# Kernel tuning notes

Measured on AMD Instinct MI355X. Metric: run time of the kernel, lower is better.

## Reference

```python
import jax, jax.numpy as jnp
import numpy as np

EPS = 1e-4

B, H, T, DH = 4, 16, 4096, 64
NF = 256


def _gaussian_orthogonal_random_matrix(rng, n_rows, n_cols):
    # Stacked orthogonal blocks from QR of gaussian blocks, scaled by row norms
    n_full = n_rows // n_cols
    blocks = []
    for _ in range(n_full):
        g = rng.standard_normal((n_cols, n_cols)).astype(np.float32)
        q, _ = np.linalg.qr(g)
        blocks.append(q.T)
    rem = n_rows - n_full * n_cols
    if rem > 0:
        g = rng.standard_normal((n_cols, n_cols)).astype(np.float32)
        q, _ = np.linalg.qr(g)
        blocks.append(q.T[:rem])
    final = np.concatenate(blocks, axis=0)
    multiplier = np.linalg.norm(rng.standard_normal((n_rows, n_cols)).astype(np.float32), axis=1)
    return (multiplier[:, None] * final).astype(np.float32)


def setup_inputs() -> dict:
    key = jax.random.key(0)
    kq, kk, kv = jax.random.split(key, 3)
    q = jax.random.normal(kq, (B, H, T, DH), dtype=jnp.float32)
    k = jax.random.normal(kk, (B, H, T, DH), dtype=jnp.float32)
    v = jax.random.normal(kv, (B, H, T, DH), dtype=jnp.float32)
    proj = jnp.asarray(_gaussian_orthogonal_random_matrix(np.random.default_rng(0), NF, DH))
    return {"q": q, "k": k, "v": v, "projection_matrix": proj}


def _softmax_kernel(data, proj, is_query):
    # data: [B,H,T,Dh], proj: [NF,Dh]
    data_scale = data.shape[-1] ** -0.25
    scale = proj.shape[0] ** -0.5
    dp = jnp.einsum('bhid,jd->bhij', data_scale * data, proj)  # [B,H,T,NF]
    dn = (jnp.sum(data ** 2, axis=-1) * (0.5 * data_scale ** 2))[..., None]
    axes = (-1, -2) if is_query else (-1,)
    m = jax.lax.stop_gradient(jnp.max(dp, axis=axes, keepdims=True))
    return scale * jnp.exp(dp - dn - m + EPS)


def reference(q, k, v, projection_matrix):
    qp = _softmax_kernel(q, projection_matrix, True)   # [B,H,T,NF]
    kp = _softmax_kernel(k, projection_matrix, False)  # [B,H,T,NF]
    context = jnp.einsum('bhnd,bhne->bhde', kp, v)     # [B,H,NF,Dh]
    d_inv = 1.0 / jnp.einsum('bhnd,bhd->bhn', qp, kp.sum(axis=-2))
    out = jnp.einsum('bhde,bhnd,bhn->bhne', context, qp, d_inv)
    return out
```

## Files before the change

kernel.cpp:

```cpp
#include <hip/hip_runtime.h>

typedef _Float16 f16;
typedef __attribute__((ext_vector_type(4))) _Float16 f16x4;
typedef __attribute__((ext_vector_type(8))) _Float16 f16x8;
typedef __attribute__((ext_vector_type(4))) float f32x4;

#define Tn 4096
#define DHn 64
#define NFn 256
#define BHn 64
#define TCH 64
#define NCH 8
#define TBLK (TCH * NCH)
#define GRIDX (Tn / TBLK)
#define KLD 72
#define WLDA 72
#define WLDB 264
#define CTXF (65 * NFn)

static constexpr float L2E  = 1.4426950408889634f;
static constexpr float DS   = 0.35355339059327379f;
static constexpr float DSL  = 0.35355339059327379f * 1.4426950408889634f;
static constexpr float DNS2 = 0.0625f * 1.4426950408889634f;
static constexpr float SH2  = 12.0f * 1.4426950408889634f;

__device__ __forceinline__ float fexp2(float x) { return __builtin_amdgcn_exp2f(x); }

#define BAR() do { asm volatile("s_waitcnt lgkmcnt(0)" ::: "memory"); \
                   __builtin_amdgcn_s_barrier(); } while (0)

__global__ __launch_bounds__(256, 2)
void perf_ctx_mfma(const float* __restrict__ K, const float* __restrict__ V,
                   const float* __restrict__ P, float* __restrict__ ctxws,
                   float* __restrict__ part, int use_part)
{
    __shared__ __align__(16) f16 kLDS[TCH * KLD];
    __shared__ __align__(16) f16 vT[2][DHn * KLD];
    __shared__ __align__(16) f16 wLDS[NFn * WLDA];
    __shared__ float dn[TCH];
    __shared__ __align__(16) float redmax[TCH][4];

    const int bh   = blockIdx.y;
    const int tid  = threadIdx.x;
    const int lane = tid & 63;
    const int wv   = tid >> 6;
    const int c    = lane & 15;
    const int g    = lane >> 4;

    f16x8 pb[4][2];
#pragma unroll
    for (int nt = 0; nt < 4; nt++)
#pragma unroll
        for (int kc = 0; kc < 2; kc++) {
            const float* s = P + (size_t)(64 * wv + 16 * nt + c) * DHn + 32 * kc + 8 * g;
            f16x8 h;
#pragma unroll
            for (int j = 0; j < 8; j++) h[j] = (f16)(s[j] * DSL);
            pb[nt][kc] = h;
        }

    f32x4 cacc[4][4];
#pragma unroll
    for (int a = 0; a < 4; a++)
#pragma unroll
        for (int b = 0; b < 4; b++) cacc[a][b] = (f32x4){0.f, 0.f, 0.f, 0.f};
    float sp[4] = {0.f, 0.f, 0.f, 0.f};

    const float* Kb = K + (size_t)bh * Tn * DHn;
    const float* Vb = V + (size_t)bh * Tn * DHn;
    const int rb = 4 * wv + g;

    float4 kq[4], vq[4], kqn[4], vqn[4];
    {
        const int t0 = blockIdx.x * TBLK;
#pragma unroll
        for (int i = 0; i < 4; i++) {
            const int r = 16 * i + rb;
            kq[i] = *(const float4*)(Kb + (size_t)(t0 + r) * DHn + 4 * c);
            vq[i] = *(const float4*)(Vb + (size_t)(t0 + r) * DHn + 4 * c);
        }
    }

    for (int ch = 0; ch < NCH; ch++) {
        f16* vTc = &vT[ch & 1][0];
#pragma unroll
        for (int i = 0; i < 4; i++) {
            const int r = 16 * i + rb;
            f16x4 hk;
            hk[0] = (f16)kq[i].x; hk[1] = (f16)kq[i].y;
            hk[2] = (f16)kq[i].z; hk[3] = (f16)kq[i].w;
            *(f16x4*)&kLDS[r * KLD + 4 * c] = hk;
            float p = kq[i].x * kq[i].x + kq[i].y * kq[i].y +
                      kq[i].z * kq[i].z + kq[i].w * kq[i].w;
            p += __shfl_xor(p, 1); p += __shfl_xor(p, 2);
            p += __shfl_xor(p, 4); p += __shfl_xor(p, 8);
            if (c == 0) dn[r] = p * DNS2;
            const float* vf = &vq[i].x;
#pragma unroll
            for (int m = 0; m < 4; m++) {
                const int dh = 4 * c + m;
                vTc[dh * KLD + ((((r >> 3) ^ ((dh >> 3) & 7)) << 3) | (r & 7))] = (f16)vf[m];
            }
        }
        if (ch + 1 < NCH) {
            const int t1 = blockIdx.x * TBLK + (ch + 1) * TCH;
#pragma unroll
            for (int i = 0; i < 4; i++) {
                const int r = 16 * i + rb;
                kqn[i] = *(const float4*)(Kb + (size_t)(t1 + r) * DHn + 4 * c);
                vqn[i] = *(const float4*)(Vb + (size_t)(t1 + r) * DHn + 4 * c);
            }
        }
        BAR();

        f32x4 dp[4][4];
#pragma unroll
        for (int a = 0; a < 4; a++)
#pragma unroll
            for (int b = 0; b < 4; b++) dp[a][b] = (f32x4){0.f, 0.f, 0.f, 0.f};
        __builtin_amdgcn_s_setprio(1);
#pragma unroll
        for (int mt = 0; mt < 4; mt++) {
            const f16x8 a0 = *(const f16x8*)&kLDS[(16 * mt + c) * KLD + 8 * g];
            const f16x8 a1 = *(const f16x8*)&kLDS[(16 * mt + c) * KLD + 32 + 8 * g];
#pragma unroll
            for (int nt = 0; nt < 4; nt++) {
                dp[mt][nt] = __builtin_amdgcn_mfma_f32_16x16x32_f16(a0, pb[nt][0], dp[mt][nt], 0, 0, 0);
                dp[mt][nt] = __builtin_amdgcn_mfma_f32_16x16x32_f16(a1, pb[nt][1], dp[mt][nt], 0, 0, 0);
            }
        }
        __builtin_amdgcn_s_setprio(0);
#pragma unroll
        for (int mt = 0; mt < 4; mt++)
#pragma unroll
            for (int r = 0; r < 4; r++) {
                float m = fmaxf(fmaxf(dp[mt][0][r], dp[mt][1][r]),
                                fmaxf(dp[mt][2][r], dp[mt][3][r]));
                m = fmaxf(m, __shfl_xor(m, 1)); m = fmaxf(m, __shfl_xor(m, 2));
                m = fmaxf(m, __shfl_xor(m, 4)); m = fmaxf(m, __shfl_xor(m, 8));
                if (c == 0) redmax[16 * mt + 4 * g + r][wv] = m;
            }
        BAR();

#pragma unroll
        for (int mt = 0; mt < 4; mt++) {
            float mx[4];
#pragma unroll
            for (int r = 0; r < 4; r++) {
                const int t = 16 * mt + 4 * g + r;
                const f32x4 rm = *(const f32x4*)&redmax[t][0];
                mx[r] = fmaxf(fmaxf(rm[0], rm[1]), fmaxf(rm[2], rm[3])) + dn[t];
            }
#pragma unroll
            for (int nt = 0; nt < 4; nt++) {
                f16x4 hw;
#pragma unroll
                for (int r = 0; r < 4; r++) {
                    const float w = fexp2(dp[mt][nt][r] - mx[r]);
                    sp[nt] += w;
                    hw[r] = (f16)w;
                }
                *(f16x4*)&wLDS[(64 * wv + 16 * nt + c) * WLDA + 16 * mt + 4 * g] = hw;
            }
        }
        BAR();

        __builtin_amdgcn_s_setprio(1);
#pragma unroll
        for (int kc = 0; kc < 2; kc++) {
            f16x8 af[4], bf[4];
#pragma unroll
            for (int mt2 = 0; mt2 < 4; mt2++)
                af[mt2] = *(const f16x8*)&wLDS[(64 * wv + 16 * mt2 + c) * WLDA + 32 * kc + 8 * g];
#pragma unroll
            for (int nt2 = 0; nt2 < 4; nt2++) {
                const int dh = 16 * nt2 + c;
                const int tb = 4 * kc + g;
                bf[nt2] = *(const f16x8*)&vTc[dh * KLD + ((tb ^ ((dh >> 3) & 7)) << 3)];
            }
#pragma unroll
            for (int mt2 = 0; mt2 < 4; mt2++)
#pragma unroll
                for (int nt2 = 0; nt2 < 4; nt2++)
                    cacc[mt2][nt2] = __builtin_amdgcn_mfma_f32_16x16x32_f16(
                        af[mt2], bf[nt2], cacc[mt2][nt2], 0, 0, 0);
        }
        __builtin_amdgcn_s_setprio(0);
#pragma unroll
        for (int i = 0; i < 4; i++) { kq[i] = kqn[i]; vq[i] = vqn[i]; }
    }

    if (use_part) {
        float* pb2 = part + (size_t)(bh * GRIDX + blockIdx.x) * CTXF;
#pragma unroll
        for (int mt2 = 0; mt2 < 4; mt2++)
#pragma unroll
            for (int nt2 = 0; nt2 < 4; nt2++)
                *(f32x4*)&pb2[(size_t)(16 * nt2 + c) * NFn + 64 * wv + 16 * mt2 + 4 * g] =
                    cacc[mt2][nt2];
#pragma unroll
        for (int nt = 0; nt < 4; nt++) {
            float sv = sp[nt];
            sv += __shfl_xor(sv, 16); sv += __shfl_xor(sv, 32);
            if (g == 0) pb2[64 * NFn + 64 * wv + 16 * nt + c] = sv;
        }
    } else {
        float* cb = ctxws + (size_t)bh * CTXF;
#pragma unroll
        for (int mt2 = 0; mt2 < 4; mt2++)
#pragma unroll
            for (int nt2 = 0; nt2 < 4; nt2++)
#pragma unroll
                for (int r = 0; r < 4; r++)
                    atomicAdd(&cb[(size_t)(16 * nt2 + c) * NFn + 64 * wv + 16 * mt2 + 4 * g + r],
                              cacc[mt2][nt2][r]);
#pragma unroll
        for (int nt = 0; nt < 4; nt++) {
            float sv = sp[nt];
            sv += __shfl_xor(sv, 16); sv += __shfl_xor(sv, 32);
            if (g == 0) atomicAdd(&cb[64 * NFn + 64 * wv + 16 * nt + c], sv);
        }
    }
}

__global__ __launch_bounds__(256)
void perf_reduce(const float* __restrict__ part, float* __restrict__ ctxws)
{
    const int bh = blockIdx.y;
    const float* p0 = part + (size_t)bh * GRIDX * CTXF;
    float* cb = ctxws + (size_t)bh * CTXF;
    for (int j = 4 * (threadIdx.x + 256 * blockIdx.x); j < CTXF; j += 4 * 256 * 8) {
        float4 a = *(const float4*)(p0 + j);
#pragma unroll
        for (int s = 1; s < GRIDX; s++) {
            const float4 b4 = *(const float4*)(p0 + (size_t)s * CTXF + j);
            a.x += b4.x; a.y += b4.y; a.z += b4.z; a.w += b4.w;
        }
        *(float4*)(cb + j) = a;
    }
}

__global__ __launch_bounds__(256, 2)
void perf_out_mfma(const float* __restrict__ Q, const float* __restrict__ P,
                   const float* __restrict__ ctxws, float* __restrict__ Out)
{
    __shared__ __align__(16) f16 qLDS[TCH * KLD];
    __shared__ __align__(16) f16 wLDS[TCH * WLDB];
    __shared__ __align__(16) f16 ctxLDS[DHn * WLDB];
    __shared__ float sLDS[NFn];
    __shared__ __align__(16) float denP[TCH][4];

    const int bh   = blockIdx.y;
    const int tid  = threadIdx.x;
    const int lane = tid & 63;
    const int wv   = tid >> 6;
    const int c    = lane & 15;
    const int g    = lane >> 4;

    const float* Qb = Q + (size_t)bh * Tn * DHn;
    float* Ob = Out + (size_t)bh * Tn * DHn;
    const int rb = 4 * wv + g;

    float4 qv[4], qvn[4];
    {
        const int t0 = blockIdx.x * TBLK;
#pragma unroll
        for (int i = 0; i < 4; i++)
            qv[i] = *(const float4*)(Qb + (size_t)(t0 + 16 * i + rb) * DHn + 4 * c);
    }

    f16x8 pb[4][2];
#pragma unroll
    for (int nt = 0; nt < 4; nt++)
#pragma unroll
        for (int kc = 0; kc < 2; kc++) {
            const float* s = P + (size_t)(64 * wv + 16 * nt + c) * DHn + 32 * kc + 8 * g;
            f16x8 h;
#pragma unroll
            for (int j = 0; j < 8; j++) h[j] = (f16)(s[j] * DSL);
            pb[nt][kc] = h;
        }

    const float* cb = ctxws + (size_t)bh * CTXF;
    {
        const int dh = tid >> 2;
        const int nq = (tid & 3) * 64;
#pragma unroll
        for (int u = 0; u < 16; u++) {
            const float4 cv = *(const float4*)&cb[(size_t)dh * NFn + nq + 4 * u];
            const float* cf = &cv.x;
#pragma unroll
            for (int i = 0; i < 4; i++) {
                const int ct = nq + 4 * u + i;
                const int cs = (ct & ~63) | ((ct & 15) << 2) | ((ct >> 4) & 3);
                ctxLDS[dh * WLDB + cs] = (f16)cf[i];
            }
        }
        sLDS[tid] = cb[64 * NFn + tid];
    }
    BAR();
    float s4[4];
#pragma unroll
    for (int nt = 0; nt < 4; nt++) s4[nt] = sLDS[64 * wv + 16 * nt + c];

    for (int ch = 0; ch < NCH; ch++) {
        const int t0 = blockIdx.x * TBLK + ch * TCH;
#pragma unroll
        for (int i = 0; i < 4; i++) {
            const int r = 16 * i + rb;
            f16x4 h;
            h[0] = (f16)qv[i].x; h[1] = (f16)qv[i].y;
            h[2] = (f16)qv[i].z; h[3] = (f16)qv[i].w;
            *(f16x4*)&qLDS[r * KLD + 4 * c] = h;
        }
        if (ch + 1 < NCH) {
            const int t1 = blockIdx.x * TBLK + (ch + 1) * TCH;
#pragma unroll
            for (int i = 0; i < 4; i++)
                qvn[i] = *(const float4*)(Qb + (size_t)(t1 + 16 * i + rb) * DHn + 4 * c);
        }
        BAR();

        f32x4 dp[4][4];
#pragma unroll
        for (int a = 0; a < 4; a++)
#pragma unroll
            for (int b = 0; b < 4; b++) dp[a][b] = (f32x4){0.f, 0.f, 0.f, 0.f};
        __builtin_amdgcn_s_setprio(1);
#pragma unroll
        for (int mt = 0; mt < 4; mt++) {
            const f16x8 a0 = *(const f16x8*)&qLDS[(16 * mt + c) * KLD + 8 * g];
            const f16x8 a1 = *(const f16x8*)&qLDS[(16 * mt + c) * KLD + 32 + 8 * g];
#pragma unroll
            for (int nt = 0; nt < 4; nt++) {
                dp[mt][nt] = __builtin_amdgcn_mfma_f32_16x16x32_f16(a0, pb[nt][0], dp[mt][nt], 0, 0, 0);
                dp[mt][nt] = __builtin_amdgcn_mfma_f32_16x16x32_f16(a1, pb[nt][1], dp[mt][nt], 0, 0, 0);
            }
        }
        __builtin_amdgcn_s_setprio(0);

#pragma unroll
        for (int mt = 0; mt < 4; mt++) {
#pragma unroll
            for (int r = 0; r < 4; r++) {
                const float w0 = fexp2(dp[mt][0][r] - SH2);
                const float w1 = fexp2(dp[mt][1][r] - SH2);
                const float w2 = fexp2(dp[mt][2][r] - SH2);
                const float w3 = fexp2(dp[mt][3][r] - SH2);
                float d = w0 * s4[0] + w1 * s4[1] + w2 * s4[2] + w3 * s4[3];
                d += __shfl_xor(d, 1); d += __shfl_xor(d, 2);
                d += __shfl_xor(d, 4); d += __shfl_xor(d, 8);
                const int t = 16 * mt + 4 * g + r;
                if (c == 0) denP[t][wv] = d;
                f16x4 hw;
                hw[0] = (f16)w0; hw[1] = (f16)w1; hw[2] = (f16)w2; hw[3] = (f16)w3;
                *(f16x4*)&wLDS[t * WLDB + 64 * wv + 4 * c] = hw;
            }
        }
        BAR();

        f32x4 oacc[4];
#pragma unroll
        for (int nt2 = 0; nt2 < 4; nt2++) oacc[nt2] = (f32x4){0.f, 0.f, 0.f, 0.f};
        __builtin_amdgcn_s_setprio(1);
#pragma unroll
        for (int kc = 0; kc < 8; kc++) {
            const f16x8 a = *(const f16x8*)&wLDS[(16 * wv + c) * WLDB + 32 * kc + 8 * g];
#pragma unroll
            for (int nt2 = 0; nt2 < 4; nt2++) {
                const f16x8 b = *(const f16x8*)&ctxLDS[(16 * nt2 + c) * WLDB + 32 * kc + 8 * g];
                oacc[nt2] = __builtin_amdgcn_mfma_f32_16x16x32_f16(a, b, oacc[nt2], 0, 0, 0);
            }
        }
        __builtin_amdgcn_s_setprio(0);
#pragma unroll
        for (int r = 0; r < 4; r++) {
            const int t = 16 * wv + 4 * g + r;
            const f32x4 d4 = *(const f32x4*)&denP[t][0];
            const float dinv = __builtin_amdgcn_rcpf(d4[0] + d4[1] + d4[2] + d4[3]);
#pragma unroll
            for (int nt2 = 0; nt2 < 4; nt2++)
                Ob[(size_t)(t0 + t) * DHn + 16 * nt2 + c] = oacc[nt2][r] * dinv;
        }
        BAR();
#pragma unroll
        for (int i = 0; i < 4; i++) qv[i] = qvn[i];
    }
}

extern "C" void kernel_launch(void* const* d_in, const int* in_sizes, int n_in,
                              void* d_out, int out_size, void* d_ws, size_t ws_size,
                              hipStream_t stream) {
    const float* q    = (const float*)d_in[0];
    const float* k    = (const float*)d_in[1];
    const float* v    = (const float*)d_in[2];
    const float* proj = (const float*)d_in[3];
    float* out = (float*)d_out;
    float* ctx = (float*)d_ws;

    (void)in_sizes; (void)n_in; (void)out_size;

    const size_t ctx_bytes  = (size_t)BHn * CTXF * sizeof(float);
    const size_t part_bytes = (size_t)BHn * GRIDX * CTXF * sizeof(float);
    const int use_part = (ws_size >= ctx_bytes + part_bytes) ? 1 : 0;
    float* part = ctx + (size_t)BHn * CTXF;

    if (!use_part)
        hipMemsetAsync(ctx, 0, ctx_bytes, stream);
    perf_ctx_mfma<<<dim3(GRIDX, BHn), 256, 0, stream>>>(k, v, proj, ctx, part, use_part);
    if (use_part)
        perf_reduce<<<dim3(8, BHn), 256, 0, stream>>>(part, ctx);
    perf_out_mfma<<<dim3(GRIDX, BHn), 256, 0, stream>>>(q, proj, ctx, out);
}
```

Measured before the change: 268.6 us.

## Double workgroup size to 8 waves, splitting feature columns across waves

```diff
diff --git a/kernel.cpp b/kernel.cpp
--- a/kernel.cpp
+++ b/kernel.cpp
@@ -1,6 +1,7 @@
 #include <hip/hip_runtime.h>
 
 typedef _Float16 f16;
+typedef __attribute__((ext_vector_type(2))) _Float16 f16x2;
 typedef __attribute__((ext_vector_type(4))) _Float16 f16x4;
 typedef __attribute__((ext_vector_type(8))) _Float16 f16x8;
 typedef __attribute__((ext_vector_type(4))) float f32x4;
@@ -18,8 +19,6 @@
 #define WLDB 264
 #define CTXF (65 * NFn)
 
-static constexpr float L2E  = 1.4426950408889634f;
-static constexpr float DS   = 0.35355339059327379f;
 static constexpr float DSL  = 0.35355339059327379f * 1.4426950408889634f;
 static constexpr float DNS2 = 0.0625f * 1.4426950408889634f;
 static constexpr float SH2  = 12.0f * 1.4426950408889634f;
@@ -29,7 +28,7 @@
 #define BAR() do { asm volatile("s_waitcnt lgkmcnt(0)" ::: "memory"); \
                    __builtin_amdgcn_s_barrier(); } while (0)
 
-__global__ __launch_bounds__(256, 2)
+__global__ __launch_bounds__(512, 4)
 void perf_ctx_mfma(const float* __restrict__ K, const float* __restrict__ V,
                    const float* __restrict__ P, float* __restrict__ ctxws,
                    float* __restrict__ part, int use_part)
@@ -38,7 +37,7 @@
     __shared__ __align__(16) f16 vT[2][DHn * KLD];
     __shared__ __align__(16) f16 wLDS[NFn * WLDA];
     __shared__ float dn[TCH];
-    __shared__ __align__(16) float redmax[TCH][4];
+    __shared__ __align__(16) float redmax[TCH][8];
 
     const int bh   = blockIdx.y;
     const int tid  = threadIdx.x;
@@ -47,35 +46,35 @@
     const int c    = lane & 15;
     const int g    = lane >> 4;
 
-    f16x8 pb[4][2];
-#pragma unroll
-    for (int nt = 0; nt < 4; nt++)
+    f16x8 pb[2][2];
+#pragma unroll
+    for (int nt = 0; nt < 2; nt++)
 #pragma unroll
         for (int kc = 0; kc < 2; kc++) {
-            const float* s = P + (size_t)(64 * wv + 16 * nt + c) * DHn + 32 * kc + 8 * g;
+            const float* s = P + (size_t)(32 * wv + 16 * nt + c) * DHn + 32 * kc + 8 * g;
             f16x8 h;
 #pragma unroll
             for (int j = 0; j < 8; j++) h[j] = (f16)(s[j] * DSL);
             pb[nt][kc] = h;
         }
 
-    f32x4 cacc[4][4];
-#pragma unroll
-    for (int a = 0; a < 4; a++)
+    f32x4 cacc[2][4];
+#pragma unroll
+    for (int a = 0; a < 2; a++)
 #pragma unroll
         for (int b = 0; b < 4; b++) cacc[a][b] = (f32x4){0.f, 0.f, 0.f, 0.f};
-    float sp[4] = {0.f, 0.f, 0.f, 0.f};
+    float sp[2] = {0.f, 0.f};
 
     const float* Kb = K + (size_t)bh * Tn * DHn;
     const float* Vb = V + (size_t)bh * Tn * DHn;
-    const int rb = 4 * wv + g;
-
-    float4 kq[4], vq[4], kqn[4], vqn[4];
+    const int rb = tid >> 4;
+
+    float4 kq[2], vq[2], kqn[2], vqn[2];
     {
         const int t0 = blockIdx.x * TBLK;
 #pragma unroll
-        for (int i = 0; i < 4; i++) {
-            const int r = 16 * i + rb;
+        for (int i = 0; i < 2; i++) {
+            const int r = 32 * i + rb;
             kq[i] = *(const float4*)(Kb + (size_t)(t0 + r) * DHn + 4 * c);
             vq[i] = *(const float4*)(Vb + (size_t)(t0 + r) * DHn + 4 * c);
         }
@@ -84,8 +83,8 @@
     for (int ch = 0; ch < NCH; ch++) {
         f16* vTc = &vT[ch & 1][0];
 #pragma unroll
-        for (int i = 0; i < 4; i++) {
-            const int r = 16 * i + rb;
+        for (int i = 0; i < 2; i++) {
+            const int r = 32 * i + rb;
             f16x4 hk;
             hk[0] = (f16)kq[i].x; hk[1] = (f16)kq[i].y;
             hk[2] = (f16)kq[i].z; hk[3] = (f16)kq[i].w;
@@ -105,26 +104,26 @@
         if (ch + 1 < NCH) {
             const int t1 = blockIdx.x * TBLK + (ch + 1) * TCH;
 #pragma unroll
-            for (int i = 0; i < 4; i++) {
-                const int r = 16 * i + rb;
+            for (int i = 0; i < 2; i++) {
+                const int r = 32 * i + rb;
                 kqn[i] = *(const float4*)(Kb + (size_t)(t1 + r) * DHn + 4 * c);
                 vqn[i] = *(const float4*)(Vb + (size_t)(t1 + r) * DHn + 4 * c);
             }
         }
         BAR();
 
-        f32x4 dp[4][4];
+        f32x4 dp[4][2];
 #pragma unroll
         for (int a = 0; a < 4; a++)
 #pragma unroll
-            for (int b = 0; b < 4; b++) dp[a][b] = (f32x4){0.f, 0.f, 0.f, 0.f};
+            for (int b = 0; b < 2; b++) dp[a][b] = (f32x4){0.f, 0.f, 0.f, 0.f};
         __builtin_amdgcn_s_setprio(1);
 #pragma unroll
         for (int mt = 0; mt < 4; mt++) {
             const f16x8 a0 = *(const f16x8*)&kLDS[(16 * mt + c) * KLD + 8 * g];
             const f16x8 a1 = *(const f16x8*)&kLDS[(16 * mt + c) * KLD + 32 + 8 * g];
 #pragma unroll
-            for (int nt = 0; nt < 4; nt++) {
+            for (int nt = 0; nt < 2; nt++) {
                 dp[mt][nt] = __builtin_amdgcn_mfma_f32_16x16x32_f16(a0, pb[nt][0], dp[mt][nt], 0, 0, 0);
                 dp[mt][nt] = __builtin_amdgcn_mfma_f32_16x16x32_f16(a1, pb[nt][1], dp[mt][nt], 0, 0, 0);
             }
@@ -134,8 +133,7 @@
         for (int mt = 0; mt < 4; mt++)
 #pragma unroll
             for (int r = 0; r < 4; r++) {
-                float m = fmaxf(fmaxf(dp[mt][0][r], dp[mt][1][r]),
-                                fmaxf(dp[mt][2][r], dp[mt][3][r]));
+                float m = fmaxf(dp[mt][0][r], dp[mt][1][r]);
                 m = fmaxf(m, __shfl_xor(m, 1)); m = fmaxf(m, __shfl_xor(m, 2));
                 m = fmaxf(m, __shfl_xor(m, 4)); m = fmaxf(m, __shfl_xor(m, 8));
                 if (c == 0) redmax[16 * mt + 4 * g + r][wv] = m;
@@ -148,11 +146,13 @@
 #pragma unroll
             for (int r = 0; r < 4; r++) {
                 const int t = 16 * mt + 4 * g + r;
-                const f32x4 rm = *(const f32x4*)&redmax[t][0];
-                mx[r] = fmaxf(fmaxf(rm[0], rm[1]), fmaxf(rm[2], rm[3])) + dn[t];
-            }
-#pragma unroll
-            for (int nt = 0; nt < 4; nt++) {
+                const f32x4 r0 = *(const f32x4*)&redmax[t][0];
+                const f32x4 r1 = *(const f32x4*)&redmax[t][4];
+                mx[r] = fmaxf(fmaxf(fmaxf(r0[0], r0[1]), fmaxf(r0[2], r0[3])),
+                              fmaxf(fmaxf(r1[0], r1[1]), fmaxf(r1[2], r1[3]))) + dn[t];
+            }
+#pragma unroll
+            for (int nt = 0; nt < 2; nt++) {
                 f16x4 hw;
 #pragma unroll
                 for (int r = 0; r < 4; r++) {
@@ -160,7 +160,7 @@
                     sp[nt] += w;
                     hw[r] = (f16)w;
                 }
-                *(f16x4*)&wLDS[(64 * wv + 16 * nt + c) * WLDA + 16 * mt + 4 * g] = hw;
+                *(f16x4*)&wLDS[(32 * wv + 16 * nt + c) * WLDA + 16 * mt + 4 * g] = hw;
             }
         }
         BAR();
@@ -168,10 +168,10 @@
         __builtin_amdgcn_s_setprio(1);
 #pragma unroll
         for (int kc = 0; kc < 2; kc++) {
-            f16x8 af[4], bf[4];
-#pragma unroll
-            for (int mt2 = 0; mt2 < 4; mt2++)
-                af[mt2] = *(const f16x8*)&wLDS[(64 * wv + 16 * mt2 + c) * WLDA + 32 * kc + 8 * g];
+            f16x8 af[2], bf[4];
+#pragma unroll
+            for (int mt2 = 0; mt2 < 2; mt2++)
+                af[mt2] = *(const f16x8*)&wLDS[(32 * wv + 16 * mt2 + c) * WLDA + 32 * kc + 8 * g];
 #pragma unroll
             for (int nt2 = 0; nt2 < 4; nt2++) {
                 const int dh = 16 * nt2 + c;
@@ -179,7 +179,7 @@
                 bf[nt2] = *(const f16x8*)&vTc[dh * KLD + ((tb ^ ((dh >> 3) & 7)) << 3)];
             }
 #pragma unroll
-            for (int mt2 = 0; mt2 < 4; mt2++)
+            for (int mt2 = 0; mt2 < 2; mt2++)
 #pragma unroll
                 for (int nt2 = 0; nt2 < 4; nt2++)
                     cacc[mt2][nt2] = __builtin_amdgcn_mfma_f32_16x16x32_f16(
@@ -187,38 +187,38 @@
         }
         __builtin_amdgcn_s_setprio(0);
 #pragma unroll
-        for (int i = 0; i < 4; i++) { kq[i] = kqn[i]; vq[i] = vqn[i]; }
+        for (int i = 0; i < 2; i++) { kq[i] = kqn[i]; vq[i] = vqn[i]; }
     }
 
     if (use_part) {
         float* pb2 = part + (size_t)(bh * GRIDX + blockIdx.x) * CTXF;
 #pragma unroll
-        for (int mt2 = 0; mt2 < 4; mt2++)
+        for (int mt2 = 0; mt2 < 2; mt2++)
 #pragma unroll
             for (int nt2 = 0; nt2 < 4; nt2++)
-                *(f32x4*)&pb2[(size_t)(16 * nt2 + c) * NFn + 64 * wv + 16 * mt2 + 4 * g] =
+                *(f32x4*)&pb2[(size_t)(16 * nt2 + c) * NFn + 32 * wv + 16 * mt2 + 4 * g] =
                     cacc[mt2][nt2];
 #pragma unroll
-        for (int nt = 0; nt < 4; nt++) {
+        for (int nt = 0; nt < 2; nt++) {
             float sv = sp[nt];
             sv += __shfl_xor(sv, 16); sv += __shfl_xor(sv, 32);
-            if (g == 0) pb2[64 * NFn + 64 * wv + 16 * nt + c] = sv;
+            if (g == 0) pb2[64 * NFn + 32 * wv + 16 * nt + c] = sv;
         }
     } else {
         float* cb = ctxws + (size_t)bh * CTXF;
 #pragma unroll
-        for (int mt2 = 0; mt2 < 4; mt2++)
+        for (int mt2 = 0; mt2 < 2; mt2++)
 #pragma unroll
             for (int nt2 = 0; nt2 < 4; nt2++)
 #pragma unroll
                 for (int r = 0; r < 4; r++)
-                    atomicAdd(&cb[(size_t)(16 * nt2 + c) * NFn + 64 * wv + 16 * mt2 + 4 * g + r],
+                    atomicAdd(&cb[(size_t)(16 * nt2 + c) * NFn + 32 * wv + 16 * mt2 + 4 * g + r],
                               cacc[mt2][nt2][r]);
 #pragma unroll
-        for (int nt = 0; nt < 4; nt++) {
+        for (int nt = 0; nt < 2; nt++) {
             float sv = sp[nt];
             sv += __shfl_xor(sv, 16); sv += __shfl_xor(sv, 32);
-            if (g == 0) atomicAdd(&cb[64 * NFn + 64 * wv + 16 * nt + c], sv);
+            if (g == 0) atomicAdd(&cb[64 * NFn + 32 * wv + 16 * nt + c], sv);
         }
     }
 }
@@ -240,7 +240,7 @@
     }
 }
 
-__global__ __launch_bounds__(256, 2)
+__global__ __launch_bounds__(512, 4)
 void perf_out_mfma(const float* __restrict__ Q, const float* __restrict__ P,
                    const float* __restrict__ ctxws, float* __restrict__ Out)
 {
@@ -248,7 +248,7 @@
     __shared__ __align__(16) f16 wLDS[TCH * WLDB];
     __shared__ __align__(16) f16 ctxLDS[DHn * WLDB];
     __shared__ float sLDS[NFn];
-    __shared__ __align__(16) float denP[TCH][4];
+    __shared__ __align__(16) float denP[TCH][8];
 
     const int bh   = blockIdx.y;
     const int tid  = threadIdx.x;
@@ -259,22 +259,22 @@
 
     const float* Qb = Q + (size_t)bh * Tn * DHn;
     float* Ob = Out + (size_t)bh * Tn * DHn;
-    const int rb = 4 * wv + g;
-
-    float4 qv[4], qvn[4];
+    const int rb = tid >> 4;
+
+    float4 qv[2], qvn[2];
     {
         const int t0 = blockIdx.x * TBLK;
 #pragma unroll
-        for (int i = 0; i < 4; i++)
-            qv[i] = *(const float4*)(Qb + (size_t)(t0 + 16 * i + rb) * DHn + 4 * c);
-    }
-
-    f16x8 pb[4][2];
-#pragma unroll
-    for (int nt = 0; nt < 4; nt++)
+        for (int i = 0; i < 2; i++)
+            qv[i] = *(const float4*)(Qb + (size_t)(t0 + 32 * i + rb) * DHn + 4 * c);
+    }
+
+    f16x8 pb[2][2];
+#pragma unroll
+    for (int nt = 0; nt < 2; nt++)
 #pragma unroll
         for (int kc = 0; kc < 2; kc++) {
-            const float* s = P + (size_t)(64 * wv + 16 * nt + c) * DHn + 32 * kc + 8 * g;
+            const float* s = P + (size_t)(32 * wv + 16 * nt + c) * DHn + 32 * kc + 8 * g;
             f16x8 h;
 #pragma unroll
             for (int j = 0; j < 8; j++) h[j] = (f16)(s[j] * DSL);
@@ -283,31 +283,34 @@
 
     const float* cb = ctxws + (size_t)bh * CTXF;
     {
-        const int dh = tid >> 2;
-        const int nq = (tid & 3) * 64;
-#pragma unroll
-        for (int u = 0; u < 16; u++) {
+        const int dh = tid >> 3;
+        const int nq = (tid & 7) * 32;
+#pragma unroll
+        for (int u = 0; u < 8; u++) {
             const float4 cv = *(const float4*)&cb[(size_t)dh * NFn + nq + 4 * u];
             const float* cf = &cv.x;
 #pragma unroll
             for (int i = 0; i < 4; i++) {
                 const int ct = nq + 4 * u + i;
-                const int cs = (ct & ~63) | ((ct & 15) << 2) | ((ct >> 4) & 3);
+                const int cs = (ct & ~31) | ((ct & 15) << 1) | ((ct >> 4) & 1);
                 ctxLDS[dh * WLDB + cs] = (f16)cf[i];
             }
         }
-        sLDS[tid] = cb[64 * NFn + tid];
+        if (tid < NFn) sLDS[tid] = cb[64 * NFn + tid];
     }
     BAR();
-    float s4[4];
-#pragma unroll
-    for (int nt = 0; nt < 4; nt++) s4[nt] = sLDS[64 * wv + 16 * nt + c];
+    float s4[2];
+#pragma unroll
+    for (int nt = 0; nt < 2; nt++) s4[nt] = sLDS[32 * wv + 16 * nt + c];
+
+    const int mtw = wv & 3;
+    const int nhw = wv >> 2;
 
     for (int ch = 0; ch < NCH; ch++) {
         const int t0 = blockIdx.x * TBLK + ch * TCH;
 #pragma unroll
-        for (int i = 0; i < 4; i++) {
-            const int r = 16 * i + rb;
+        for (int i = 0; i < 2; i++) {
+            const int r = 32 * i + rb;
             f16x4 h;
             h[0] = (f16)qv[i].x; h[1] = (f16)qv[i].y;
             h[2] = (f16)qv[i].z; h[3] = (f16)qv[i].w;
@@ -316,23 +319,23 @@
         if (ch + 1 < NCH) {
             const int t1 = blockIdx.x * TBLK + (ch + 1) * TCH;
 #pragma unroll
-            for (int i = 0; i < 4; i++)
-                qvn[i] = *(const float4*)(Qb + (size_t)(t1 + 16 * i + rb) * DHn + 4 * c);
-        }
-        BAR();
-
-        f32x4 dp[4][4];
+            for (int i = 0; i < 2; i++)
+                qvn[i] = *(const float4*)(Qb + (size_t)(t1 + 32 * i + rb) * DHn + 4 * c);
+        }
+        BAR();
+
+        f32x4 dp[4][2];
 #pragma unroll
         for (int a = 0; a < 4; a++)
 #pragma unroll
-            for (int b = 0; b < 4; b++) dp[a][b] = (f32x4){0.f, 0.f, 0.f, 0.f};
+            for (int b = 0; b < 2; b++) dp[a][b] = (f32x4){0.f, 0.f, 0.f, 0.f};
         __builtin_amdgcn_s_setprio(1);
 #pragma unroll
         for (int mt = 0; mt < 4; mt++) {
             const f16x8 a0 = *(const f16x8*)&qLDS[(16 * mt + c) * KLD + 8 * g];
             const f16x8 a1 = *(const f16x8*)&qLDS[(16 * mt + c) * KLD + 32 + 8 * g];
 #pragma unroll
-            for (int nt = 0; nt < 4; nt++) {
+            for (int nt = 0; nt < 2; nt++) {
                 dp[mt][nt] = __builtin_amdgcn_mfma_f32_16x16x32_f16(a0, pb[nt][0], dp[mt][nt], 0, 0, 0);
                 dp[mt][nt] = __builtin_amdgcn_mfma_f32_16x16x32_f16(a1, pb[nt][1], dp[mt][nt], 0, 0, 0);
             }
@@ -345,46 +348,47 @@
             for (int r = 0; r < 4; r++) {
                 const float w0 = fexp2(dp[mt][0][r] - SH2);
                 const float w1 = fexp2(dp[mt][1][r] - SH2);
-                const float w2 = fexp2(dp[mt][2][r] - SH2);
-                const float w3 = fexp2(dp[mt][3][r] - SH2);
-                float d = w0 * s4[0] + w1 * s4[1] + w2 * s4[2] + w3 * s4[3];
+                float d = w0 * s4[0] + w1 * s4[1];
                 d += __shfl_xor(d, 1); d += __shfl_xor(d, 2);
                 d += __shfl_xor(d, 4); d += __shfl_xor(d, 8);
                 const int t = 16 * mt + 4 * g + r;
                 if (c == 0) denP[t][wv] = d;
-                f16x4 hw;
-                hw[0] = (f16)w0; hw[1] = (f16)w1; hw[2] = (f16)w2; hw[3] = (f16)w3;
-                *(f16x4*)&wLDS[t * WLDB + 64 * wv + 4 * c] = hw;
-            }
-        }
-        BAR();
-
-        f32x4 oacc[4];
-#pragma unroll
-        for (int nt2 = 0; nt2 < 4; nt2++) oacc[nt2] = (f32x4){0.f, 0.f, 0.f, 0.f};
+                f16x2 hw;
+                hw[0] = (f16)w0; hw[1] = (f16)w1;
+                *(f16x2*)&wLDS[t * WLDB + 32 * wv + 2 * c] = hw;
+            }
+        }
+        BAR();
+
+        f32x4 oacc[2];
+#pragma unroll
+        for (int j = 0; j < 2; j++) oacc[j] = (f32x4){0.f, 0.f, 0.f, 0.f};
         __builtin_amdgcn_s_setprio(1);
 #pragma unroll
         for (int kc = 0; kc < 8; kc++) {
-            const f16x8 a = *(const f16x8*)&wLDS[(16 * wv + c) * WLDB + 32 * kc + 8 * g];
-#pragma unroll
-            for (int nt2 = 0; nt2 < 4; nt2++) {
+            const f16x8 a = *(const f16x8*)&wLDS[(16 * mtw + c) * WLDB + 32 * kc + 8 * g];
+#pragma unroll
+            for (int j = 0; j < 2; j++) {
+                const int nt2 = 2 * nhw + j;
                 const f16x8 b = *(const f16x8*)&ctxLDS[(16 * nt2 + c) * WLDB + 32 * kc + 8 * g];
-                oacc[nt2] = __builtin_amdgcn_mfma_f32_16x16x32_f16(a, b, oacc[nt2], 0, 0, 0);
+                oacc[j] = __builtin_amdgcn_mfma_f32_16x16x32_f16(a, b, oacc[j], 0, 0, 0);
             }
         }
         __builtin_amdgcn_s_setprio(0);
 #pragma unroll
         for (int r = 0; r < 4; r++) {
-            const int t = 16 * wv + 4 * g + r;
-            const f32x4 d4 = *(const f32x4*)&denP[t][0];
-            const float dinv = __builtin_amdgcn_rcpf(d4[0] + d4[1] + d4[2] + d4[3]);
-#pragma unroll
-            for (int nt2 = 0; nt2 < 4; nt2++)
-                Ob[(size_t)(t0 + t) * DHn + 16 * nt2 + c] = oacc[nt2][r] * dinv;
-        }
-        BAR();
-#pragma unroll
-        for (int i = 0; i < 4; i++) qv[i] = qvn[i];
+            const int t = 16 * mtw + 4 * g + r;
+            const f32x4 d0 = *(const f32x4*)&denP[t][0];
+            const f32x4 d1 = *(const f32x4*)&denP[t][4];
+            const float dinv = __builtin_amdgcn_rcpf(
+                (d0[0] + d0[1] + d0[2] + d0[3]) + (d1[0] + d1[1] + d1[2] + d1[3]));
+#pragma unroll
+            for (int j = 0; j < 2; j++)
+                Ob[(size_t)(t0 + t) * DHn + 16 * (2 * nhw + j) + c] = oacc[j][r] * dinv;
+        }
+        BAR();
+#pragma unroll
+        for (int i = 0; i < 2; i++) qv[i] = qvn[i];
     }
 }
 
@@ -407,8 +411,8 @@
 
     if (!use_part)
         hipMemsetAsync(ctx, 0, ctx_bytes, stream);
-    perf_ctx_mfma<<<dim3(GRIDX, BHn), 256, 0, stream>>>(k, v, proj, ctx, part, use_part);
+    perf_ctx_mfma<<<dim3(GRIDX, BHn), 512, 0, stream>>>(k, v, proj, ctx, part, use_part);
     if (use_part)
         perf_reduce<<<dim3(8, BHn), 256, 0, stream>>>(part, ctx);
-    perf_out_mfma<<<dim3(GRIDX, BHn), 256, 0, stream>>>(q, proj, ctx, out);
+    perf_out_mfma<<<dim3(GRIDX, BHn), 512, 0, stream>>>(q, proj, ctx, out);
 }
```

New measurement: 328.5 us. 1.22x slower.
